# Performance work log

Hardware: AMD Instinct MI355X
Metric: run time of the kernel (lower is better)

The kernel has to match this reference:

```python
import jax, jax.numpy as jnp
import numpy as np

NW, NT, ND = 100000, 20000, 5000      # wallet / token / dev node counts
DW, DT, DD = 32, 32, 16               # raw feature dims
H = 64                                 # GATConv out channels (heads=1)
E_WW, E_BU, E_SE, E_CR = 1600000, 1000000, 1000000, 20000


def setup_inputs() -> dict:
    key = jax.random.key(0)
    ks = iter(jax.random.split(key, 80))

    def nrm(shape, s=1.0):
        return jax.random.normal(next(ks), shape, dtype=jnp.float32) * s

    inp = {
        "x_wallet": nrm((NW, DW)),
        "x_token": nrm((NT, DT)),
        "x_dev": nrm((ND, DD)),
    }
    # per-relation GATConv params: lin_src, lin_dst (bias=False), att_src, att_dst, bias
    rels = [("g1ww", DW, DW), ("g1bu", DW, DT), ("g1se", DW, DT), ("g1cr", DD, DT),
            ("g2ww", H, H), ("g2bu", H, H), ("g2se", H, H)]
    for pre, ds, dd in rels:
        inp[pre + "_Ws"] = nrm((ds, H), 0.1)
        inp[pre + "_Wd"] = nrm((dd, H), 0.1)
        inp[pre + "_as"] = nrm((H,), 0.1)
        inp[pre + "_ad"] = nrm((H,), 0.1)
        inp[pre + "_b"] = nrm((H,), 0.1)
    inp["Wfc"] = nrm((H, 2), 0.1)
    inp["bfc"] = nrm((2,), 0.1)

    for name, n, hi in [("ww_src", E_WW, NW), ("ww_dst", E_WW, NW),
                        ("bu_src", E_BU, NW), ("bu_dst", E_BU, NT),
                        ("se_src", E_SE, NW), ("se_dst", E_SE, NT),
                        ("cr_src", E_CR, ND), ("cr_dst", E_CR, NT)]:
        inp[name] = jax.random.randint(next(ks), (n,), 0, hi, dtype=jnp.int32)
    return inp


def gat(xs, xd, src, dst, Ws, Wd, a_s, a_d, b, n_dst):
    """PyG GATConv, heads=1, add_self_loops=False, negative_slope=0.2."""
    hs = xs @ Ws                                   # [Ns, H]
    e = jax.nn.leaky_relu((hs @ a_s)[src] + ((xd @ Wd) @ a_d)[dst], 0.2)  # [E]
    m = jax.ops.segment_max(e, dst, num_segments=n_dst)
    ex = jnp.exp(e - m[dst])
    den = jax.ops.segment_sum(ex, dst, num_segments=n_dst)
    alpha = ex / (den[dst] + 1e-16)                # scatter-softmax over dst
    out = jax.ops.segment_sum(alpha[:, None] * hs[src], dst, num_segments=n_dst)
    return out + b


def reference(x_wallet, x_token, x_dev,
              g1ww_Ws, g1ww_Wd, g1ww_as, g1ww_ad, g1ww_b,
              g1bu_Ws, g1bu_Wd, g1bu_as, g1bu_ad, g1bu_b,
              g1se_Ws, g1se_Wd, g1se_as, g1se_ad, g1se_b,
              g1cr_Ws, g1cr_Wd, g1cr_as, g1cr_ad, g1cr_b,
              g2ww_Ws, g2ww_Wd, g2ww_as, g2ww_ad, g2ww_b,
              g2bu_Ws, g2bu_Wd, g2bu_as, g2bu_ad, g2bu_b,
              g2se_Ws, g2se_Wd, g2se_as, g2se_ad, g2se_b,
              Wfc, bfc,
              ww_src, ww_dst, bu_src, bu_dst, se_src, se_dst, cr_src, cr_dst):
    # conv1 (HeteroConv, aggr='sum'): dev has no incoming edges -> dropped
    w1 = gat(x_wallet, x_wallet, ww_src, ww_dst, g1ww_Ws, g1ww_Wd, g1ww_as, g1ww_ad, g1ww_b, NW)
    t1 = (gat(x_wallet, x_token, bu_src, bu_dst, g1bu_Ws, g1bu_Wd, g1bu_as, g1bu_ad, g1bu_b, NT)
          + gat(x_wallet, x_token, se_src, se_dst, g1se_Ws, g1se_Wd, g1se_as, g1se_ad, g1se_b, NT)
          + gat(x_dev, x_token, cr_src, cr_dst, g1cr_Ws, g1cr_Wd, g1cr_as, g1cr_ad, g1cr_b, NT))
    # conv2: 'dev' absent from x_dict, so ('dev','creates','token') is skipped by HeteroConv
    w2 = gat(w1, w1, ww_src, ww_dst, g2ww_Ws, g2ww_Wd, g2ww_as, g2ww_ad, g2ww_b, NW)  # computed but unused downstream (matches torch)
    t2 = (gat(w1, t1, bu_src, bu_dst, g2bu_Ws, g2bu_Wd, g2bu_as, g2bu_ad, g2bu_b, NT)
          + gat(w1, t1, se_src, se_dst, g2se_Ws, g2se_Wd, g2se_as, g2se_ad, g2se_b, NT))
    del w2
    return t2 @ Wfc + bfc  # [NT, 2]
```

## Files before the change

kernel.cpp:

```cpp
#include <hip/hip_runtime.h>

#define NW 100000
#define NT 20000
#define ND 5000
#define EWW 1600000
#define EBU 1000000
#define ESE 1000000
#define ECR 20000
#define EPB 16384
#define SBTH 1024
#define SITER 16
#define ABTH 512

#define WWSH 8
#define WWW 256
#define NBWB 391
#define WCAP 6144
#define WITER 12
#define TSH 6
#define TW 64
#define NBTB 313
#define TCAP 4096
#define TITER 8
#define CCAP 512
#define CITER 1

typedef unsigned int uint;

#define R_EDWW 0
#define R_EDBU 1
#define R_EDSE 2
#define R_EDCR 3
#define R_WV2BU 4
#define R_WV2SE 5
#define R_ESWW 6
#define R_ESBU 7
#define R_ESSE 8
#define R_ESCR 9
#define R_WS2BU 10
#define R_WS2SE 11
#define R_VBU 12
#define R_VSE 13
#define R_DBU_B 14
#define R_DSE_B 15
#define R_DBU_S 16
#define R_DSE_S 17
#define R_DBU_C 18
#define R_DSE_C 19
#define R_TBU0 20
#define R_TBU1 21
#define R_TSE0 22
#define R_TSE1 23
#define R_CBU 24
#define R_CSE 25
#define R_SBU 26
#define R_SSE 27
#define R_MBU0 28
#define R_MBU1 29
#define R_MSE0 30
#define R_MSE1 31
#define R_CB1U0 32
#define R_CB1U1 33
#define R_CB1S0 34
#define R_CB1S1 35
#define R_C20 36
#define R_C21 37
#define R_F0 38
#define R_F1 39
#define R_BT1 40
#define R_BT2 41
#define NROWS 42


__global__ void k_scur(int* __restrict__ ccur) {
    int t = blockIdx.x * 256 + threadIdx.x;
    if (t < 4096) {
        int li = t >> 10, i = t & 1023;
        int cap = (li == 0) ? WCAP : (li == 3 ? CCAP : TCAP);
        ccur[t] = i * cap;
    }
}

__global__ __launch_bounds__(64) void k_smallprep(const float* __restrict__ Wfc,
                                                  const float* __restrict__ b1a,
                                                  const float* __restrict__ b1b,
                                                  const float* __restrict__ b1c,
                                                  const float* __restrict__ b2a,
                                                  const float* __restrict__ b2b,
                                                  float* __restrict__ wvbuf) {
    int t = threadIdx.x;
    if (blockIdx.x == 0) {
        wvbuf[R_F0 * 64 + t] = Wfc[t * 2];
        wvbuf[R_F1 * 64 + t] = Wfc[t * 2 + 1];
    } else if (blockIdx.x == 1) {
        wvbuf[R_BT1 * 64 + t] = b1a[t] + b1b[t] + b1c[t];
    } else {
        wvbuf[R_BT2 * 64 + t] = b2a[t] + b2b[t];
    }
}


struct BMeta {
    const int* src[4]; const int* dst[4];
    int* ccur[4];
    uint* pairs[4];
    int E[4]; int shift[4]; int cap[4]; int bbase[5];
};

__device__ __forceinline__ int find_list(const int* bbase, int b) {
    int li = 0;
    while (li < 3 && b >= bbase[li + 1]) ++li;
    return li;
}

__global__ __launch_bounds__(SBTH) void k_cscat4(BMeta a) {
    __shared__ int scnt[1024];
    __shared__ int sbase[1024];
    for (int i = threadIdx.x; i < 1024; i += SBTH) scnt[i] = 0;
    __syncthreads();
    int li = find_list(a.bbase, blockIdx.x);
    int lb = blockIdx.x - a.bbase[li];
    const int* src = a.src[li];
    const int* dst = a.dst[li];
    uint* pairs = a.pairs[li];
    int* ccur = a.ccur[li];
    int sh = a.shift[li];
    int cap = a.cap[li];
    uint mask = (1u << sh) - 1u;
    int b0 = lb * EPB;
    int end = min(b0 + EPB, a.E[li]);
    int t = threadIdx.x;

    uint pk[SITER];
    int bk[SITER];
    int rk[SITER];
#pragma unroll
    for (int k = 0; k < SITER; ++k) {
        int i = b0 + t + k * SBTH;
        bool v = i < end;
        int d = v ? dst[i] : 0;
        int s = v ? src[i] : 0;
        int b = d >> sh;
        pk[k] = (uint)s | (((uint)d & mask) << 20);
        rk[k] = v ? atomicAdd(&scnt[b], 1) : 0;
        bk[k] = v ? b : -1;
    }
    __syncthreads();
    for (int i = t; i < 1024; i += SBTH) {
        int c = scnt[i];
        sbase[i] = c ? atomicAdd(&ccur[i], c) : 0;
    }
    __syncthreads();
#pragma unroll
    for (int k = 0; k < SITER; ++k) {
        if (bk[k] >= 0) {
            int p = sbase[bk[k]] + rk[k];
            if (p < (bk[k] + 1) * cap)
                pairs[p] = pk[k];
        }
    }
}


struct WvN { const float* M[16]; const float* v[16]; int K[16]; };

__global__ __launch_bounds__(64) void k_wvN(WvN a, float* __restrict__ out) {
    int b = blockIdx.x, t = threadIdx.x;
    if (t < a.K[b]) {
        const float* M = a.M[b];
        const float* v = a.v[b];
        float s = 0.f;
        for (int j = 0; j < 64; ++j) s = fmaf(M[t * 64 + j], v[j], s);
        out[b * 64 + t] = s;
    }
}


struct PrepWP {
    const float* X; int N;
    const float* v[14];
    float* edww;
    float* PW; float4* TB; float4* TS;
};

__global__ __launch_bounds__(256) void k_prepw(PrepWP a) {
    int wvid = (blockIdx.x * 256 + threadIdx.x) >> 6;
    int half = (threadIdx.x >> 5) & 1;
    int l = threadIdx.x & 31;
    int r = wvid * 2 + half;
    float x = (r < a.N) ? a.X[(size_t)r * 32 + l] : 0.f;
    float p[14];
#pragma unroll
    for (int i = 0; i < 14; ++i) p[i] = x * a.v[i][l];
#pragma unroll
    for (int o = 1; o < 32; o <<= 1) {
#pragma unroll
        for (int i = 0; i < 14; ++i) p[i] += __shfl_xor(p[i], o, 64);
    }
    if (l == 0 && r < a.N) {
        a.edww[r] = p[3];
        float4* P = (float4*)(a.PW + (size_t)r * 8);
        P[0] = make_float4(p[4], p[5], p[6], p[7]);
        P[1] = make_float4(p[8], p[9], p[0], 0.f);
        a.TB[r] = make_float4(p[10], p[11], p[1], 0.f);
        a.TS[r] = make_float4(p[12], p[13], p[2], 0.f);
    }
}

struct PrepTD {
    const float* Xt; const float* Xd;
    const float* tv0; const float* tv1; const float* tv2;
    const float* dv0; const float* dv1; const float* dv2;
    float* e0; float* e1; float* e2;
    float4* TC;
    int nbT;
};

__global__ __launch_bounds__(256) void k_preptd(PrepTD a) {
    if ((int)blockIdx.x < a.nbT) {
        int wvid = (blockIdx.x * 256 + threadIdx.x) >> 6;
        int half = (threadIdx.x >> 5) & 1;
        int l = threadIdx.x & 31;
        int r = wvid * 2 + half;
        float x = (r < NT) ? a.Xt[(size_t)r * 32 + l] : 0.f;
        float p0 = x * a.tv0[l], p1 = x * a.tv1[l], p2 = x * a.tv2[l];
#pragma unroll
        for (int o = 1; o < 32; o <<= 1) {
            p0 += __shfl_xor(p0, o, 64);
            p1 += __shfl_xor(p1, o, 64);
            p2 += __shfl_xor(p2, o, 64);
        }
        if (l == 0 && r < NT) { a.e0[r] = p0; a.e1[r] = p1; a.e2[r] = p2; }
    } else {
        int grp = ((blockIdx.x - a.nbT) * 256 + threadIdx.x) >> 4;
        int l = threadIdx.x & 15;
        int r = grp;
        float x = (r < ND) ? a.Xd[(size_t)r * 16 + l] : 0.f;
        float p0 = x * a.dv0[l], p1 = x * a.dv1[l], p2 = x * a.dv2[l];
#pragma unroll
        for (int o = 1; o < 16; o <<= 1) {
            p0 += __shfl_xor(p0, o, 64);
            p1 += __shfl_xor(p1, o, 64);
            p2 += __shfl_xor(p2, o, 64);
        }
        if (l == 0 && r < ND) a.TC[r] = make_float4(p1, p2, p0, 0.f);
    }
}


template <int ITER>
__device__ __forceinline__ void sort_bucket(const uint* __restrict__ slab, int cnt,
                                            int ndl, uint* sp, int* hoff, int* hcnt,
                                            int t) {
    if (t < ndl) hcnt[t] = 0;
    __syncthreads();
    uint pk[ITER];
    int gk[ITER];
    int rk[ITER];
#pragma unroll
    for (int k = 0; k < ITER; ++k) {
        int i = t + k * ABTH;
        bool v = i < cnt;
        uint pr = v ? slab[i] : 0;
        int g = pr >> 20;
        pk[k] = pr & 0xFFFFFu;
        rk[k] = v ? atomicAdd(&hcnt[g], 1) : 0;
        gk[k] = v ? g : -1;
    }
    __syncthreads();
    int own = (t < ndl) ? hcnt[t] : 0;
    if (t < ndl) hoff[t] = own;
    __syncthreads();
    for (int o = 1; o < ndl; o <<= 1) {
        int u = 0;
        if (t < ndl && t >= o) u = hoff[t - o];
        __syncthreads();
        if (t < ndl && t >= o) hoff[t] += u;
        __syncthreads();
    }
    if (t < ndl) hoff[t] -= own;
    __syncthreads();
#pragma unroll
    for (int k = 0; k < ITER; ++k)
        if (gk[k] >= 0) sp[hoff[gk[k]] + rk[k]] = pk[k];
    __syncthreads();
}


__global__ __launch_bounds__(ABTH) void k_fsaggw(const uint* __restrict__ pairs,
                                                 const int* __restrict__ ccur,
                                                 const float* __restrict__ ed,
                                                 const float* __restrict__ PW,
                                                 const float* __restrict__ C,
                                                 float4* __restrict__ TL2B,
                                                 float4* __restrict__ TL2S) {
    __shared__ uint sp[WCAP];
    __shared__ int hoff[WWW];
    __shared__ int hcnt[WWW];
    __shared__ float eds[WWW];
    int t = threadIdx.x, b = blockIdx.x;
    int d0 = b << WWSH;
    if (t < WWW) {
        int d = d0 + t;
        eds[t] = (d < NW) ? ed[d] : 0.f;
    }
    int cnt = min(ccur[b] - b * WCAP, WCAP);
    sort_bucket<WITER>(pairs + (size_t)b * WCAP, cnt, WWW, sp, hoff, hcnt, t);
    int dl = t >> 1, sub = t & 1;
    float edj = eds[dl];
    float A0 = 0, A1 = 0, A2 = 0, A3 = 0, A4 = 0, A5 = 0, den = 0;
    int s0 = hoff[dl], s1 = s0 + hcnt[dl];
    for (int j = s0 + sub; j < s1; j += 2) {
        int s = sp[j];
        const float4* P = (const float4*)(PW + (size_t)s * 8);
        float4 u = P[0], v = P[1];
        float e = v.z + edj;
        e = e > 0.f ? e : 0.2f * e;
        float w = __expf(e);
        den += w;
        A0 = fmaf(w, u.x, A0); A1 = fmaf(w, u.y, A1); A2 = fmaf(w, u.z, A2);
        A3 = fmaf(w, u.w, A3); A4 = fmaf(w, v.x, A4); A5 = fmaf(w, v.y, A5);
    }
    A0 += __shfl_xor(A0, 1, 64); A1 += __shfl_xor(A1, 1, 64);
    A2 += __shfl_xor(A2, 1, 64); A3 += __shfl_xor(A3, 1, 64);
    A4 += __shfl_xor(A4, 1, 64); A5 += __shfl_xor(A5, 1, 64);
    den += __shfl_xor(den, 1, 64);
    if (sub == 0) {
        int d = d0 + dl;
        if (d < NW) {
            float c0 = C[R_CBU * 64], c1 = C[R_CSE * 64];
            float c2 = C[R_CB1U0 * 64], c3 = C[R_CB1U1 * 64];
            float c4 = C[R_CB1S0 * 64], c5 = C[R_CB1S1 * 64];
            if (den > 0.f) {
                float inv = 1.f / (den + 1e-16f);
                TL2B[d] = make_float4(A2 * inv + c2, A3 * inv + c3, A0 * inv + c0, 0.f);
                TL2S[d] = make_float4(A4 * inv + c4, A5 * inv + c5, A1 * inv + c1, 0.f);
            } else {
                TL2B[d] = make_float4(c2, c3, c0, 0.f);
                TL2S[d] = make_float4(c4, c5, c1, 0.f);
            }
        }
    }
}


__global__ __launch_bounds__(ABTH) void k_fsaggt(const uint* __restrict__ pB,
                                                 const uint* __restrict__ pS,
                                                 const uint* __restrict__ pC,
                                                 const int* __restrict__ curB,
                                                 const int* __restrict__ curS,
                                                 const int* __restrict__ curC,
                                                 const float* __restrict__ edB,
                                                 const float* __restrict__ edS,
                                                 const float* __restrict__ edC,
                                                 const float4* __restrict__ TB,
                                                 const float4* __restrict__ TS,
                                                 const float4* __restrict__ TC,
                                                 const float4* __restrict__ TL2B,
                                                 const float4* __restrict__ TL2S,
                                                 const float* __restrict__ C,
                                                 const float* __restrict__ bfc,
                                                 float* __restrict__ out) {
    __shared__ uint spB[TCAP];
    __shared__ uint spS[TCAP];
    __shared__ uint spC[CCAP];
    __shared__ int hoB[TW], hcB[TW], hoS[TW], hcS[TW], hoC[TW], hcC[TW];
    __shared__ float eds[3][TW];
    int t = threadIdx.x, b = blockIdx.x;
    int d0 = b << TSH;
    if (t < TW) {
        int d = d0 + t;
        eds[0][t] = (d < NT) ? edB[d] : 0.f;
        eds[1][t] = (d < NT) ? edS[d] : 0.f;
        eds[2][t] = (d < NT) ? edC[d] : 0.f;
    }
    int cntB = min(curB[b] - b * TCAP, TCAP);
    int cntS = min(curS[b] - b * TCAP, TCAP);
    int cntC = min(curC[b] - b * CCAP, CCAP);
    sort_bucket<TITER>(pB + (size_t)b * TCAP, cntB, TW, spB, hoB, hcB, t);
    sort_bucket<TITER>(pS + (size_t)b * TCAP, cntS, TW, spS, hoS, hcS, t);
    sort_bucket<CITER>(pC + (size_t)b * CCAP, cntC, TW, spC, hoC, hcC, t);

    int dl = t >> 3, sub = t & 7;

    float bx = 0, by = 0, bd = 0;
    for (int j = hoB[dl] + sub; j < hoB[dl] + hcB[dl]; j += 8) {
        float4 q = TB[spB[j]];
        float e = q.z + eds[0][dl];
        e = e > 0.f ? e : 0.2f * e;
        float w = __expf(e);
        bd += w; bx = fmaf(w, q.x, bx); by = fmaf(w, q.y, by);
    }
    float sx = 0, sy = 0, sd = 0;
    for (int j = hoS[dl] + sub; j < hoS[dl] + hcS[dl]; j += 8) {
        float4 q = TS[spS[j]];
        float e = q.z + eds[1][dl];
        e = e > 0.f ? e : 0.2f * e;
        float w = __expf(e);
        sd += w; sx = fmaf(w, q.x, sx); sy = fmaf(w, q.y, sy);
    }
    float cx = 0, cy = 0, cd = 0;
    for (int j = hoC[dl] + sub; j < hoC[dl] + hcC[dl]; j += 8) {
        float4 q = TC[spC[j]];
        float e = q.z + eds[2][dl];
        e = e > 0.f ? e : 0.2f * e;
        float w = __expf(e);
        cd += w; cx = fmaf(w, q.x, cx); cy = fmaf(w, q.y, cy);
    }
#pragma unroll
    for (int o = 1; o < 8; o <<= 1) {
        bx += __shfl_xor(bx, o, 64); by += __shfl_xor(by, o, 64); bd += __shfl_xor(bd, o, 64);
        sx += __shfl_xor(sx, o, 64); sy += __shfl_xor(sy, o, 64); sd += __shfl_xor(sd, o, 64);
        cx += __shfl_xor(cx, o, 64); cy += __shfl_xor(cy, o, 64); cd += __shfl_xor(cd, o, 64);
    }
    float qbx = 0, qby = 0, qsx = 0, qsy = 0, qcx = 0, qcy = 0;
    if (bd > 0.f) { float i = 1.f / (bd + 1e-16f); qbx = bx * i; qby = by * i; }
    if (sd > 0.f) { float i = 1.f / (sd + 1e-16f); qsx = sx * i; qsy = sy * i; }
    if (cd > 0.f) { float i = 1.f / (cd + 1e-16f); qcx = cx * i; qcy = cy * i; }
    float ed2b = C[R_SBU * 64] + qbx + qsx + qcx;
    float ed2s = C[R_SSE * 64] + qby + qsy + qcy;

    float rbx = 0, rby = 0, rbd = 0;
    for (int j = hoB[dl] + sub; j < hoB[dl] + hcB[dl]; j += 8) {
        float4 q = TL2B[spB[j]];
        float e = q.z + ed2b;
        e = e > 0.f ? e : 0.2f * e;
        float w = __expf(e);
        rbd += w; rbx = fmaf(w, q.x, rbx); rby = fmaf(w, q.y, rby);
    }
    float rsx = 0, rsy = 0, rsd = 0;
    for (int j = hoS[dl] + sub; j < hoS[dl] + hcS[dl]; j += 8) {
        float4 q = TL2S[spS[j]];
        float e = q.z + ed2s;
        e = e > 0.f ? e : 0.2f * e;
        float w = __expf(e);
        rsd += w; rsx = fmaf(w, q.x, rsx); rsy = fmaf(w, q.y, rsy);
    }
#pragma unroll
    for (int o = 1; o < 8; o <<= 1) {
        rbx += __shfl_xor(rbx, o, 64); rby += __shfl_xor(rby, o, 64); rbd += __shfl_xor(rbd, o, 64);
        rsx += __shfl_xor(rsx, o, 64); rsy += __shfl_xor(rsy, o, 64); rsd += __shfl_xor(rsd, o, 64);
    }
    if (sub == 0) {
        int d = d0 + dl;
        if (d < NT) {
            float fbx = 0, fby = 0, fsx = 0, fsy = 0;
            if (rbd > 0.f) { float i = 1.f / (rbd + 1e-16f); fbx = rbx * i; fby = rby * i; }
            if (rsd > 0.f) { float i = 1.f / (rsd + 1e-16f); fsx = rsx * i; fsy = rsy * i; }
            out[d * 2 + 0] = bfc[0] + C[R_C20 * 64] + fbx + fsx;
            out[d * 2 + 1] = bfc[1] + C[R_C21 * 64] + fby + fsy;
        }
    }
}


extern "C" void kernel_launch(void* const* d_in, const int* in_sizes, int n_in,
                              void* d_out, int out_size, void* d_ws, size_t ws_size,
                              hipStream_t stream) {
    const float* xw = (const float*)d_in[0];
    const float* xt = (const float*)d_in[1];
    const float* xd = (const float*)d_in[2];
    const float* g1ww_Ws = (const float*)d_in[3];
    const float* g1ww_Wd = (const float*)d_in[4];
    const float* g1ww_as = (const float*)d_in[5];
    const float* g1ww_ad = (const float*)d_in[6];
    const float* g1ww_b  = (const float*)d_in[7];
    const float* g1bu_Ws = (const float*)d_in[8];
    const float* g1bu_Wd = (const float*)d_in[9];
    const float* g1bu_as = (const float*)d_in[10];
    const float* g1bu_ad = (const float*)d_in[11];
    const float* g1bu_b  = (const float*)d_in[12];
    const float* g1se_Ws = (const float*)d_in[13];
    const float* g1se_Wd = (const float*)d_in[14];
    const float* g1se_as = (const float*)d_in[15];
    const float* g1se_ad = (const float*)d_in[16];
    const float* g1se_b  = (const float*)d_in[17];
    const float* g1cr_Ws = (const float*)d_in[18];
    const float* g1cr_Wd = (const float*)d_in[19];
    const float* g1cr_as = (const float*)d_in[20];
    const float* g1cr_ad = (const float*)d_in[21];
    const float* g1cr_b  = (const float*)d_in[22];
    const float* g2bu_Ws = (const float*)d_in[28];
    const float* g2bu_Wd = (const float*)d_in[29];
    const float* g2bu_as = (const float*)d_in[30];
    const float* g2bu_ad = (const float*)d_in[31];
    const float* g2bu_b  = (const float*)d_in[32];
    const float* g2se_Ws = (const float*)d_in[33];
    const float* g2se_Wd = (const float*)d_in[34];
    const float* g2se_as = (const float*)d_in[35];
    const float* g2se_ad = (const float*)d_in[36];
    const float* g2se_b  = (const float*)d_in[37];
    const float* Wfc = (const float*)d_in[38];
    const float* bfc = (const float*)d_in[39];
    const int* ww_src = (const int*)d_in[40];
    const int* ww_dst = (const int*)d_in[41];
    const int* bu_src = (const int*)d_in[42];
    const int* bu_dst = (const int*)d_in[43];
    const int* se_src = (const int*)d_in[44];
    const int* se_dst = (const int*)d_in[45];
    const int* cr_src = (const int*)d_in[46];
    const int* cr_dst = (const int*)d_in[47];

    char* p = (char*)d_ws;
    auto alloc = [&](size_t bytes) {
        char* r = p;
        p += (bytes + 255) & ~(size_t)255;
        return r;
    };
    uint* pairsW = (uint*)alloc((size_t)NBWB * WCAP * 4);
    uint* pairsB = (uint*)alloc((size_t)NBTB * TCAP * 4);
    uint* pairsS = (uint*)alloc((size_t)NBTB * TCAP * 4);
    uint* pairsC = (uint*)alloc((size_t)NBTB * CCAP * 4);
    int* ccur = (int*)alloc(4 * 1024 * 4);

    float* wvbuf = (float*)alloc(NROWS * 64 * 4);

    float* edww = (float*)alloc((size_t)NW * 4);
    float* edbu = (float*)alloc((size_t)NT * 4);
    float* edse = (float*)alloc((size_t)NT * 4);
    float* edcr = (float*)alloc((size_t)NT * 4);
    float* PW   = (float*)alloc((size_t)NW * 8 * 4);
    float4* TB  = (float4*)alloc((size_t)NW * 16);
    float4* TS  = (float4*)alloc((size_t)NW * 16);
    float4* TC  = (float4*)alloc((size_t)ND * 16);
    float4* TL2B = (float4*)alloc((size_t)NW * 16);
    float4* TL2S = (float4*)alloc((size_t)NW * 16);

    const int thr = 256;
    const int nbW_e = (EWW + EPB - 1) / EPB;
    const int nbB_e = (EBU + EPB - 1) / EPB;
    const int nbS_e = (ESE + EPB - 1) / EPB;
    const int nbC_e = (ECR + EPB - 1) / EPB;
    const int nbTot = nbW_e + nbB_e + nbS_e + nbC_e;

    k_scur<<<16, thr, 0, stream>>>(ccur);

    BMeta bm;
    bm.src[0] = ww_src; bm.dst[0] = ww_dst; bm.ccur[0] = ccur + 0 * 1024;
    bm.pairs[0] = pairsW; bm.E[0] = EWW; bm.shift[0] = WWSH; bm.cap[0] = WCAP;
    bm.src[1] = bu_src; bm.dst[1] = bu_dst; bm.ccur[1] = ccur + 1 * 1024;
    bm.pairs[1] = pairsB; bm.E[1] = EBU; bm.shift[1] = TSH; bm.cap[1] = TCAP;
    bm.src[2] = se_src; bm.dst[2] = se_dst; bm.ccur[2] = ccur + 2 * 1024;
    bm.pairs[2] = pairsS; bm.E[2] = ESE; bm.shift[2] = TSH; bm.cap[2] = TCAP;
    bm.src[3] = cr_src; bm.dst[3] = cr_dst; bm.ccur[3] = ccur + 3 * 1024;
    bm.pairs[3] = pairsC; bm.E[3] = ECR; bm.shift[3] = TSH; bm.cap[3] = CCAP;
    bm.bbase[0] = 0; bm.bbase[1] = nbW_e; bm.bbase[2] = nbW_e + nbB_e;
    bm.bbase[3] = nbW_e + nbB_e + nbS_e; bm.bbase[4] = nbTot;
    k_cscat4<<<nbTot, SBTH, 0, stream>>>(bm);

    k_smallprep<<<3, 64, 0, stream>>>(Wfc, g1bu_b, g1se_b, g1cr_b, g2bu_b, g2se_b, wvbuf);

    WvN A;
    A.M[0] = g1ww_Wd; A.v[0] = g1ww_ad; A.K[0] = 32;
    A.M[1] = g1bu_Wd; A.v[1] = g1bu_ad; A.K[1] = 32;
    A.M[2] = g1se_Wd; A.v[2] = g1se_ad; A.K[2] = 32;
    A.M[3] = g1cr_Wd; A.v[3] = g1cr_ad; A.K[3] = 32;
    A.M[4] = g2bu_Wd; A.v[4] = g2bu_ad; A.K[4] = 64;
    A.M[5] = g2se_Wd; A.v[5] = g2se_ad; A.K[5] = 64;
    A.M[6] = g1ww_Ws; A.v[6] = g1ww_as; A.K[6] = 32;
    A.M[7] = g1bu_Ws; A.v[7] = g1bu_as; A.K[7] = 32;
    A.M[8] = g1se_Ws; A.v[8] = g1se_as; A.K[8] = 32;
    A.M[9] = g1cr_Ws; A.v[9] = g1cr_as; A.K[9] = 16;
    A.M[10] = g2bu_Ws; A.v[10] = g2bu_as; A.K[10] = 64;
    A.M[11] = g2se_Ws; A.v[11] = g2se_as; A.K[11] = 64;
    for (int i = 12; i < 16; ++i) { A.M[i] = nullptr; A.v[i] = nullptr; A.K[i] = 0; }
    k_wvN<<<12, 64, 0, stream>>>(A, wvbuf + 0 * 64);

    WvN B;
    B.M[0] = g1ww_Ws; B.v[0] = wvbuf + R_WS2BU * 64; B.K[0] = 32;
    B.M[1] = g1ww_Ws; B.v[1] = wvbuf + R_WS2SE * 64; B.K[1] = 32;
    B.M[2] = g1bu_Ws; B.v[2] = wvbuf + R_WV2BU * 64; B.K[2] = 32;
    B.M[3] = g1bu_Ws; B.v[3] = wvbuf + R_WV2SE * 64; B.K[3] = 32;
    B.M[4] = g1se_Ws; B.v[4] = wvbuf + R_WV2BU * 64; B.K[4] = 32;
    B.M[5] = g1se_Ws; B.v[5] = wvbuf + R_WV2SE * 64; B.K[5] = 32;
    B.M[6] = g1cr_Ws; B.v[6] = wvbuf + R_WV2BU * 64; B.K[6] = 16;
    B.M[7] = g1cr_Ws; B.v[7] = wvbuf + R_WV2SE * 64; B.K[7] = 16;
    B.M[8] = g2bu_Ws; B.v[8] = wvbuf + R_F0 * 64; B.K[8] = 64;
    B.M[9] = g2bu_Ws; B.v[9] = wvbuf + R_F1 * 64; B.K[9] = 64;
    B.M[10] = g2se_Ws; B.v[10] = wvbuf + R_F0 * 64; B.K[10] = 64;
    B.M[11] = g2se_Ws; B.v[11] = wvbuf + R_F1 * 64; B.K[11] = 64;
    B.M[12] = g1ww_b; B.v[12] = wvbuf + R_WS2BU * 64; B.K[12] = 1;
    B.M[13] = g1ww_b; B.v[13] = wvbuf + R_WS2SE * 64; B.K[13] = 1;
    B.M[14] = wvbuf + R_BT1 * 64; B.v[14] = wvbuf + R_WV2BU * 64; B.K[14] = 1;
    B.M[15] = wvbuf + R_BT1 * 64; B.v[15] = wvbuf + R_WV2SE * 64; B.K[15] = 1;
    k_wvN<<<16, 64, 0, stream>>>(B, wvbuf + R_VBU * 64);

    WvN Cc;
    Cc.M[0] = g1ww_Ws; Cc.v[0] = wvbuf + R_TBU0 * 64; Cc.K[0] = 32;
    Cc.M[1] = g1ww_Ws; Cc.v[1] = wvbuf + R_TBU1 * 64; Cc.K[1] = 32;
    Cc.M[2] = g1ww_Ws; Cc.v[2] = wvbuf + R_TSE0 * 64; Cc.K[2] = 32;
    Cc.M[3] = g1ww_Ws; Cc.v[3] = wvbuf + R_TSE1 * 64; Cc.K[3] = 32;
    Cc.M[4] = g1ww_b; Cc.v[4] = wvbuf + R_TBU0 * 64; Cc.K[4] = 1;
    Cc.M[5] = g1ww_b; Cc.v[5] = wvbuf + R_TBU1 * 64; Cc.K[5] = 1;
    Cc.M[6] = g1ww_b; Cc.v[6] = wvbuf + R_TSE0 * 64; Cc.K[6] = 1;
    Cc.M[7] = g1ww_b; Cc.v[7] = wvbuf + R_TSE1 * 64; Cc.K[7] = 1;
    Cc.M[8] = wvbuf + R_BT2 * 64; Cc.v[8] = wvbuf + R_F0 * 64; Cc.K[8] = 1;
    Cc.M[9] = wvbuf + R_BT2 * 64; Cc.v[9] = wvbuf + R_F1 * 64; Cc.K[9] = 1;
    for (int i = 10; i < 16; ++i) { Cc.M[i] = nullptr; Cc.v[i] = nullptr; Cc.K[i] = 0; }
    k_wvN<<<10, 64, 0, stream>>>(Cc, wvbuf + R_MBU0 * 64);

    PrepWP pw;
    pw.X = xw; pw.N = NW;
    pw.v[0] = wvbuf + R_ESWW * 64; pw.v[1] = wvbuf + R_ESBU * 64;
    pw.v[2] = wvbuf + R_ESSE * 64; pw.v[3] = wvbuf + R_EDWW * 64;
    pw.v[4] = wvbuf + R_VBU * 64;  pw.v[5] = wvbuf + R_VSE * 64;
    pw.v[6] = wvbuf + R_MBU0 * 64; pw.v[7] = wvbuf + R_MBU1 * 64;
    pw.v[8] = wvbuf + R_MSE0 * 64; pw.v[9] = wvbuf + R_MSE1 * 64;
    pw.v[10] = wvbuf + R_DBU_B * 64; pw.v[11] = wvbuf + R_DSE_B * 64;
    pw.v[12] = wvbuf + R_DBU_S * 64; pw.v[13] = wvbuf + R_DSE_S * 64;
    pw.edww = edww;
    pw.PW = PW; pw.TB = TB; pw.TS = TS;
    k_prepw<<<(NW + 7) / 8, thr, 0, stream>>>(pw);

    PrepTD ptd;
    ptd.Xt = xt; ptd.Xd = xd;
    ptd.tv0 = wvbuf + R_EDBU * 64; ptd.tv1 = wvbuf + R_EDSE * 64; ptd.tv2 = wvbuf + R_EDCR * 64;
    ptd.dv0 = wvbuf + R_ESCR * 64; ptd.dv1 = wvbuf + R_DBU_C * 64; ptd.dv2 = wvbuf + R_DSE_C * 64;
    ptd.e0 = edbu; ptd.e1 = edse; ptd.e2 = edcr;
    ptd.TC = TC;
    ptd.nbT = (NT + 7) / 8;
    k_preptd<<<ptd.nbT + (ND + 15) / 16, thr, 0, stream>>>(ptd);

    k_fsaggw<<<NBWB, ABTH, 0, stream>>>(pairsW, ccur + 0 * 1024, edww, PW, wvbuf,
                                        TL2B, TL2S);

    k_fsaggt<<<NBTB, ABTH, 0, stream>>>(pairsB, pairsS, pairsC,
                                        ccur + 1 * 1024, ccur + 2 * 1024, ccur + 3 * 1024,
                                        edbu, edse, edcr,
                                        TB, TS, TC, TL2B, TL2S,
                                        wvbuf, bfc, (float*)d_out);
}
```

Measured before the change: 295.9 us.

## Fuse init kernels and merge edge scatter with node prep into one launch

Result: faster. 273.6 us (-7.6%).

```diff
diff --git a/kernel.cpp b/kernel.cpp
--- a/kernel.cpp
+++ b/kernel.cpp
@@ -8,7 +8,7 @@
 #define ESE 1000000
 #define ECR 20000
 #define EPB 16384
-#define SBTH 1024
+#define BBTH 1024
 #define SITER 16
 #define ABTH 512
 
@@ -71,98 +71,46 @@
 #define R_BT2 41
 #define NROWS 42
 
-
-__global__ void k_scur(int* __restrict__ ccur) {
-    int t = blockIdx.x * 256 + threadIdx.x;
-    if (t < 4096) {
-        int li = t >> 10, i = t & 1023;
+struct WvN { const float* M[16]; const float* v[16]; int K[16]; };
+
+
+struct Init1 {
+    WvN A;
+    const float* Wfc;
+    const float* b1a; const float* b1b; const float* b1c;
+    const float* b2a; const float* b2b;
+    int* ccur;
+    float* wvbuf;
+};
+
+__global__ __launch_bounds__(256) void k_init1(Init1 a) {
+    int bi = blockIdx.x, t = threadIdx.x;
+    if (bi < 16) {
+        int i = bi * 256 + t;
+        int li = i >> 10, j = i & 1023;
         int cap = (li == 0) ? WCAP : (li == 3 ? CCAP : TCAP);
-        ccur[t] = i * cap;
-    }
-}
-
-__global__ __launch_bounds__(64) void k_smallprep(const float* __restrict__ Wfc,
-                                                  const float* __restrict__ b1a,
-                                                  const float* __restrict__ b1b,
-                                                  const float* __restrict__ b1c,
-                                                  const float* __restrict__ b2a,
-                                                  const float* __restrict__ b2b,
-                                                  float* __restrict__ wvbuf) {
-    int t = threadIdx.x;
-    if (blockIdx.x == 0) {
-        wvbuf[R_F0 * 64 + t] = Wfc[t * 2];
-        wvbuf[R_F1 * 64 + t] = Wfc[t * 2 + 1];
-    } else if (blockIdx.x == 1) {
-        wvbuf[R_BT1 * 64 + t] = b1a[t] + b1b[t] + b1c[t];
+        a.ccur[i] = j * cap;
+    } else if (bi == 16) {
+        if (t < 64) {
+            a.wvbuf[R_F0 * 64 + t] = a.Wfc[t * 2];
+            a.wvbuf[R_F1 * 64 + t] = a.Wfc[t * 2 + 1];
+        }
+    } else if (bi == 17) {
+        if (t < 64) a.wvbuf[R_BT1 * 64 + t] = a.b1a[t] + a.b1b[t] + a.b1c[t];
+    } else if (bi == 18) {
+        if (t < 64) a.wvbuf[R_BT2 * 64 + t] = a.b2a[t] + a.b2b[t];
     } else {
-        wvbuf[R_BT2 * 64 + t] = b2a[t] + b2b[t];
-    }
-}
-
-
-struct BMeta {
-    const int* src[4]; const int* dst[4];
-    int* ccur[4];
-    uint* pairs[4];
-    int E[4]; int shift[4]; int cap[4]; int bbase[5];
-};
-
-__device__ __forceinline__ int find_list(const int* bbase, int b) {
-    int li = 0;
-    while (li < 3 && b >= bbase[li + 1]) ++li;
-    return li;
-}
-
-__global__ __launch_bounds__(SBTH) void k_cscat4(BMeta a) {
-    __shared__ int scnt[1024];
-    __shared__ int sbase[1024];
-    for (int i = threadIdx.x; i < 1024; i += SBTH) scnt[i] = 0;
-    __syncthreads();
-    int li = find_list(a.bbase, blockIdx.x);
-    int lb = blockIdx.x - a.bbase[li];
-    const int* src = a.src[li];
-    const int* dst = a.dst[li];
-    uint* pairs = a.pairs[li];
-    int* ccur = a.ccur[li];
-    int sh = a.shift[li];
-    int cap = a.cap[li];
-    uint mask = (1u << sh) - 1u;
-    int b0 = lb * EPB;
-    int end = min(b0 + EPB, a.E[li]);
-    int t = threadIdx.x;
-
-    uint pk[SITER];
-    int bk[SITER];
-    int rk[SITER];
-#pragma unroll
-    for (int k = 0; k < SITER; ++k) {
-        int i = b0 + t + k * SBTH;
-        bool v = i < end;
-        int d = v ? dst[i] : 0;
-        int s = v ? src[i] : 0;
-        int b = d >> sh;
-        pk[k] = (uint)s | (((uint)d & mask) << 20);
-        rk[k] = v ? atomicAdd(&scnt[b], 1) : 0;
-        bk[k] = v ? b : -1;
-    }
-    __syncthreads();
-    for (int i = t; i < 1024; i += SBTH) {
-        int c = scnt[i];
-        sbase[i] = c ? atomicAdd(&ccur[i], c) : 0;
-    }
-    __syncthreads();
-#pragma unroll
-    for (int k = 0; k < SITER; ++k) {
-        if (bk[k] >= 0) {
-            int p = sbase[bk[k]] + rk[k];
-            if (p < (bk[k] + 1) * cap)
-                pairs[p] = pk[k];
-        }
-    }
-}
-
-
-struct WvN { const float* M[16]; const float* v[16]; int K[16]; };
+        int b = bi - 19;
+        if (t < a.A.K[b]) {
+            const float* M = a.A.M[b];
+            const float* v = a.A.v[b];
+            float s = 0.f;
+            for (int j = 0; j < 64; ++j) s = fmaf(M[t * 64 + j], v[j], s);
+            a.wvbuf[b * 64 + t] = s;
+        }
+    }
+}
+
 
 __global__ __launch_bounds__(64) void k_wvN(WvN a, float* __restrict__ out) {
     int b = blockIdx.x, t = threadIdx.x;
@@ -176,51 +124,106 @@
 }
 
 
-struct PrepWP {
-    const float* X; int N;
-    const float* v[14];
-    float* edww;
-    float* PW; float4* TB; float4* TS;
+struct BMeta {
+    const int* src[4]; const int* dst[4];
+    int* ccur[4];
+    uint* pairs[4];
+    int E[4]; int shift[4]; int cap[4]; int bbase[5];
 };
 
-__global__ __launch_bounds__(256) void k_prepw(PrepWP a) {
-    int wvid = (blockIdx.x * 256 + threadIdx.x) >> 6;
-    int half = (threadIdx.x >> 5) & 1;
-    int l = threadIdx.x & 31;
-    int r = wvid * 2 + half;
-    float x = (r < a.N) ? a.X[(size_t)r * 32 + l] : 0.f;
-    float p[14];
-#pragma unroll
-    for (int i = 0; i < 14; ++i) p[i] = x * a.v[i][l];
-#pragma unroll
-    for (int o = 1; o < 32; o <<= 1) {
-#pragma unroll
-        for (int i = 0; i < 14; ++i) p[i] += __shfl_xor(p[i], o, 64);
-    }
-    if (l == 0 && r < a.N) {
-        a.edww[r] = p[3];
-        float4* P = (float4*)(a.PW + (size_t)r * 8);
-        P[0] = make_float4(p[4], p[5], p[6], p[7]);
-        P[1] = make_float4(p[8], p[9], p[0], 0.f);
-        a.TB[r] = make_float4(p[10], p[11], p[1], 0.f);
-        a.TS[r] = make_float4(p[12], p[13], p[2], 0.f);
-    }
-}
-
-struct PrepTD {
+struct Build {
+    BMeta bm;
+    const float* Xw;
+    const float* vw[14];
+    float* edww; float* PW; float4* TBt; float4* TSt;
     const float* Xt; const float* Xd;
     const float* tv0; const float* tv1; const float* tv2;
     const float* dv0; const float* dv1; const float* dv2;
     float* e0; float* e1; float* e2;
     float4* TC;
-    int nbT;
+    int nbScat, nbPW, nbPT;
 };
 
-__global__ __launch_bounds__(256) void k_preptd(PrepTD a) {
-    if ((int)blockIdx.x < a.nbT) {
-        int wvid = (blockIdx.x * 256 + threadIdx.x) >> 6;
-        int half = (threadIdx.x >> 5) & 1;
-        int l = threadIdx.x & 31;
+__device__ __forceinline__ int find_list(const int* bbase, int b) {
+    int li = 0;
+    while (li < 3 && b >= bbase[li + 1]) ++li;
+    return li;
+}
+
+__global__ __launch_bounds__(BBTH) void k_build(Build a) {
+    int t = threadIdx.x;
+    if ((int)blockIdx.x < a.nbScat) {
+        __shared__ int scnt[1024];
+        __shared__ int sbase[1024];
+        for (int i = t; i < 1024; i += BBTH) scnt[i] = 0;
+        __syncthreads();
+        int li = find_list(a.bm.bbase, blockIdx.x);
+        int lb = blockIdx.x - a.bm.bbase[li];
+        const int* src = a.bm.src[li];
+        const int* dst = a.bm.dst[li];
+        uint* pairs = a.bm.pairs[li];
+        int* ccur = a.bm.ccur[li];
+        int sh = a.bm.shift[li];
+        int cap = a.bm.cap[li];
+        uint mask = (1u << sh) - 1u;
+        int b0 = lb * EPB;
+        int end = min(b0 + EPB, a.bm.E[li]);
+        uint pk[SITER];
+        int bk[SITER];
+        int rk[SITER];
+#pragma unroll
+        for (int k = 0; k < SITER; ++k) {
+            int i = b0 + t + k * BBTH;
+            bool v = i < end;
+            int d = v ? dst[i] : 0;
+            int s = v ? src[i] : 0;
+            int b = d >> sh;
+            pk[k] = (uint)s | (((uint)d & mask) << 20);
+            rk[k] = v ? atomicAdd(&scnt[b], 1) : 0;
+            bk[k] = v ? b : -1;
+        }
+        __syncthreads();
+        for (int i = t; i < 1024; i += BBTH) {
+            int c = scnt[i];
+            sbase[i] = c ? atomicAdd(&ccur[i], c) : 0;
+        }
+        __syncthreads();
+#pragma unroll
+        for (int k = 0; k < SITER; ++k) {
+            if (bk[k] >= 0) {
+                int p = sbase[bk[k]] + rk[k];
+                if (p < (bk[k] + 1) * cap)
+                    pairs[p] = pk[k];
+            }
+        }
+    } else if ((int)blockIdx.x < a.nbScat + a.nbPW) {
+        int bid = blockIdx.x - a.nbScat;
+        int wvid = (bid * BBTH + t) >> 6;
+        int half = (t >> 5) & 1;
+        int l = t & 31;
+        int r = wvid * 2 + half;
+        float x = (r < NW) ? a.Xw[(size_t)r * 32 + l] : 0.f;
+        float p[14];
+#pragma unroll
+        for (int i = 0; i < 14; ++i) p[i] = x * a.vw[i][l];
+#pragma unroll
+        for (int o = 1; o < 32; o <<= 1) {
+#pragma unroll
+            for (int i = 0; i < 14; ++i) p[i] += __shfl_xor(p[i], o, 64);
+        }
+        if (l == 0 && r < NW) {
+            a.edww[r] = p[3];
+            float4* P = (float4*)(a.PW + (size_t)r * 8);
+            P[0] = make_float4(p[4], p[5], p[6], p[7]);
+            P[1] = make_float4(p[8], p[9], p[0], 0.f);
+            a.TBt[r] = make_float4(p[10], p[11], p[1], 0.f);
+            a.TSt[r] = make_float4(p[12], p[13], p[2], 0.f);
+        }
+    } else if ((int)blockIdx.x < a.nbScat + a.nbPW + a.nbPT) {
+        int bid = blockIdx.x - a.nbScat - a.nbPW;
+        int wvid = (bid * BBTH + t) >> 6;
+        int half = (t >> 5) & 1;
+        int l = t & 31;
         int r = wvid * 2 + half;
         float x = (r < NT) ? a.Xt[(size_t)r * 32 + l] : 0.f;
         float p0 = x * a.tv0[l], p1 = x * a.tv1[l], p2 = x * a.tv2[l];
@@ -232,9 +235,9 @@
         }
         if (l == 0 && r < NT) { a.e0[r] = p0; a.e1[r] = p1; a.e2[r] = p2; }
     } else {
-        int grp = ((blockIdx.x - a.nbT) * 256 + threadIdx.x) >> 4;
-        int l = threadIdx.x & 15;
-        int r = grp;
+        int bid = blockIdx.x - a.nbScat - a.nbPW - a.nbPT;
+        int r = (bid * BBTH + t) >> 4;
+        int l = t & 15;
         float x = (r < ND) ? a.Xd[(size_t)r * 16 + l] : 0.f;
         float p0 = x * a.dv0[l], p1 = x * a.dv1[l], p2 = x * a.dv2[l];
 #pragma unroll
@@ -526,45 +529,35 @@
     float4* TL2B = (float4*)alloc((size_t)NW * 16);
     float4* TL2S = (float4*)alloc((size_t)NW * 16);
 
-    const int thr = 256;
     const int nbW_e = (EWW + EPB - 1) / EPB;
     const int nbB_e = (EBU + EPB - 1) / EPB;
     const int nbS_e = (ESE + EPB - 1) / EPB;
     const int nbC_e = (ECR + EPB - 1) / EPB;
-    const int nbTot = nbW_e + nbB_e + nbS_e + nbC_e;
-
-    k_scur<<<16, thr, 0, stream>>>(ccur);
-
-    BMeta bm;
-    bm.src[0] = ww_src; bm.dst[0] = ww_dst; bm.ccur[0] = ccur + 0 * 1024;
-    bm.pairs[0] = pairsW; bm.E[0] = EWW; bm.shift[0] = WWSH; bm.cap[0] = WCAP;
-    bm.src[1] = bu_src; bm.dst[1] = bu_dst; bm.ccur[1] = ccur + 1 * 1024;
-    bm.pairs[1] = pairsB; bm.E[1] = EBU; bm.shift[1] = TSH; bm.cap[1] = TCAP;
-    bm.src[2] = se_src; bm.dst[2] = se_dst; bm.ccur[2] = ccur + 2 * 1024;
-    bm.pairs[2] = pairsS; bm.E[2] = ESE; bm.shift[2] = TSH; bm.cap[2] = TCAP;
-    bm.src[3] = cr_src; bm.dst[3] = cr_dst; bm.ccur[3] = ccur + 3 * 1024;
-    bm.pairs[3] = pairsC; bm.E[3] = ECR; bm.shift[3] = TSH; bm.cap[3] = CCAP;
-    bm.bbase[0] = 0; bm.bbase[1] = nbW_e; bm.bbase[2] = nbW_e + nbB_e;
-    bm.bbase[3] = nbW_e + nbB_e + nbS_e; bm.bbase[4] = nbTot;
-    k_cscat4<<<nbTot, SBTH, 0, stream>>>(bm);
-
-    k_smallprep<<<3, 64, 0, stream>>>(Wfc, g1bu_b, g1se_b, g1cr_b, g2bu_b, g2se_b, wvbuf);
-
-    WvN A;
-    A.M[0] = g1ww_Wd; A.v[0] = g1ww_ad; A.K[0] = 32;
-    A.M[1] = g1bu_Wd; A.v[1] = g1bu_ad; A.K[1] = 32;
-    A.M[2] = g1se_Wd; A.v[2] = g1se_ad; A.K[2] = 32;
-    A.M[3] = g1cr_Wd; A.v[3] = g1cr_ad; A.K[3] = 32;
-    A.M[4] = g2bu_Wd; A.v[4] = g2bu_ad; A.K[4] = 64;
-    A.M[5] = g2se_Wd; A.v[5] = g2se_ad; A.K[5] = 64;
-    A.M[6] = g1ww_Ws; A.v[6] = g1ww_as; A.K[6] = 32;
-    A.M[7] = g1bu_Ws; A.v[7] = g1bu_as; A.K[7] = 32;
-    A.M[8] = g1se_Ws; A.v[8] = g1se_as; A.K[8] = 32;
-    A.M[9] = g1cr_Ws; A.v[9] = g1cr_as; A.K[9] = 16;
-    A.M[10] = g2bu_Ws; A.v[10] = g2bu_as; A.K[10] = 64;
-    A.M[11] = g2se_Ws; A.v[11] = g2se_as; A.K[11] = 64;
-    for (int i = 12; i < 16; ++i) { A.M[i] = nullptr; A.v[i] = nullptr; A.K[i] = 0; }
-    k_wvN<<<12, 64, 0, stream>>>(A, wvbuf + 0 * 64);
+    const int nbScat = nbW_e + nbB_e + nbS_e + nbC_e;
+    const int nbPW = (NW + 31) / 32;
+    const int nbPT = (NT + 31) / 32;
+    const int nbPD = (ND + 63) / 64;
+
+    Init1 i1;
+    i1.A.M[0] = g1ww_Wd; i1.A.v[0] = g1ww_ad; i1.A.K[0] = 32;
+    i1.A.M[1] = g1bu_Wd; i1.A.v[1] = g1bu_ad; i1.A.K[1] = 32;
+    i1.A.M[2] = g1se_Wd; i1.A.v[2] = g1se_ad; i1.A.K[2] = 32;
+    i1.A.M[3] = g1cr_Wd; i1.A.v[3] = g1cr_ad; i1.A.K[3] = 32;
+    i1.A.M[4] = g2bu_Wd; i1.A.v[4] = g2bu_ad; i1.A.K[4] = 64;
+    i1.A.M[5] = g2se_Wd; i1.A.v[5] = g2se_ad; i1.A.K[5] = 64;
+    i1.A.M[6] = g1ww_Ws; i1.A.v[6] = g1ww_as; i1.A.K[6] = 32;
+    i1.A.M[7] = g1bu_Ws; i1.A.v[7] = g1bu_as; i1.A.K[7] = 32;
+    i1.A.M[8] = g1se_Ws; i1.A.v[8] = g1se_as; i1.A.K[8] = 32;
+    i1.A.M[9] = g1cr_Ws; i1.A.v[9] = g1cr_as; i1.A.K[9] = 16;
+    i1.A.M[10] = g2bu_Ws; i1.A.v[10] = g2bu_as; i1.A.K[10] = 64;
+    i1.A.M[11] = g2se_Ws; i1.A.v[11] = g2se_as; i1.A.K[11] = 64;
+    for (int i = 12; i < 16; ++i) { i1.A.M[i] = nullptr; i1.A.v[i] = nullptr; i1.A.K[i] = 0; }
+    i1.Wfc = Wfc;
+    i1.b1a = g1bu_b; i1.b1b = g1se_b; i1.b1c = g1cr_b;
+    i1.b2a = g2bu_b; i1.b2b = g2se_b;
+    i1.ccur = ccur;
+    i1.wvbuf = wvbuf;
+    k_init1<<<31, 256, 0, stream>>>(i1);
 
     WvN B;
     B.M[0] = g1ww_Ws; B.v[0] = wvbuf + R_WS2BU * 64; B.K[0] = 32;
@@ -599,27 +592,33 @@
     for (int i = 10; i < 16; ++i) { Cc.M[i] = nullptr; Cc.v[i] = nullptr; Cc.K[i] = 0; }
     k_wvN<<<10, 64, 0, stream>>>(Cc, wvbuf + R_MBU0 * 64);
 
-    PrepWP pw;
-    pw.X = xw; pw.N = NW;
-    pw.v[0] = wvbuf + R_ESWW * 64; pw.v[1] = wvbuf + R_ESBU * 64;
-    pw.v[2] = wvbuf + R_ESSE * 64; pw.v[3] = wvbuf + R_EDWW * 64;
-    pw.v[4] = wvbuf + R_VBU * 64;  pw.v[5] = wvbuf + R_VSE * 64;
-    pw.v[6] = wvbuf + R_MBU0 * 64; pw.v[7] = wvbuf + R_MBU1 * 64;
-    pw.v[8] = wvbuf + R_MSE0 * 64; pw.v[9] = wvbuf + R_MSE1 * 64;
-    pw.v[10] = wvbuf + R_DBU_B * 64; pw.v[11] = wvbuf + R_DSE_B * 64;
-    pw.v[12] = wvbuf + R_DBU_S * 64; pw.v[13] = wvbuf + R_DSE_S * 64;
-    pw.edww = edww;
-    pw.PW = PW; pw.TB = TB; pw.TS = TS;
-    k_prepw<<<(NW + 7) / 8, thr, 0, stream>>>(pw);
-
-    PrepTD ptd;
-    ptd.Xt = xt; ptd.Xd = xd;
-    ptd.tv0 = wvbuf + R_EDBU * 64; ptd.tv1 = wvbuf + R_EDSE * 64; ptd.tv2 = wvbuf + R_EDCR * 64;
-    ptd.dv0 = wvbuf + R_ESCR * 64; ptd.dv1 = wvbuf + R_DBU_C * 64; ptd.dv2 = wvbuf + R_DSE_C * 64;
-    ptd.e0 = edbu; ptd.e1 = edse; ptd.e2 = edcr;
-    ptd.TC = TC;
-    ptd.nbT = (NT + 7) / 8;
-    k_preptd<<<ptd.nbT + (ND + 15) / 16, thr, 0, stream>>>(ptd);
+    Build bd;
+    bd.bm.src[0] = ww_src; bd.bm.dst[0] = ww_dst; bd.bm.ccur[0] = ccur + 0 * 1024;
+    bd.bm.pairs[0] = pairsW; bd.bm.E[0] = EWW; bd.bm.shift[0] = WWSH; bd.bm.cap[0] = WCAP;
+    bd.bm.src[1] = bu_src; bd.bm.dst[1] = bu_dst; bd.bm.ccur[1] = ccur + 1 * 1024;
+    bd.bm.pairs[1] = pairsB; bd.bm.E[1] = EBU; bd.bm.shift[1] = TSH; bd.bm.cap[1] = TCAP;
+    bd.bm.src[2] = se_src; bd.bm.dst[2] = se_dst; bd.bm.ccur[2] = ccur + 2 * 1024;
+    bd.bm.pairs[2] = pairsS; bd.bm.E[2] = ESE; bd.bm.shift[2] = TSH; bd.bm.cap[2] = TCAP;
+    bd.bm.src[3] = cr_src; bd.bm.dst[3] = cr_dst; bd.bm.ccur[3] = ccur + 3 * 1024;
+    bd.bm.pairs[3] = pairsC; bd.bm.E[3] = ECR; bd.bm.shift[3] = TSH; bd.bm.cap[3] = CCAP;
+    bd.bm.bbase[0] = 0; bd.bm.bbase[1] = nbW_e; bd.bm.bbase[2] = nbW_e + nbB_e;
+    bd.bm.bbase[3] = nbW_e + nbB_e + nbS_e; bd.bm.bbase[4] = nbScat;
+    bd.Xw = xw;
+    bd.vw[0] = wvbuf + R_ESWW * 64; bd.vw[1] = wvbuf + R_ESBU * 64;
+    bd.vw[2] = wvbuf + R_ESSE * 64; bd.vw[3] = wvbuf + R_EDWW * 64;
+    bd.vw[4] = wvbuf + R_VBU * 64;  bd.vw[5] = wvbuf + R_VSE * 64;
+    bd.vw[6] = wvbuf + R_MBU0 * 64; bd.vw[7] = wvbuf + R_MBU1 * 64;
+    bd.vw[8] = wvbuf + R_MSE0 * 64; bd.vw[9] = wvbuf + R_MSE1 * 64;
+    bd.vw[10] = wvbuf + R_DBU_B * 64; bd.vw[11] = wvbuf + R_DSE_B * 64;
+    bd.vw[12] = wvbuf + R_DBU_S * 64; bd.vw[13] = wvbuf + R_DSE_S * 64;
+    bd.edww = edww; bd.PW = PW; bd.TBt = TB; bd.TSt = TS;
+    bd.Xt = xt; bd.Xd = xd;
+    bd.tv0 = wvbuf + R_EDBU * 64; bd.tv1 = wvbuf + R_EDSE * 64; bd.tv2 = wvbuf + R_EDCR * 64;
+    bd.dv0 = wvbuf + R_ESCR * 64; bd.dv1 = wvbuf + R_DBU_C * 64; bd.dv2 = wvbuf + R_DSE_C * 64;
+    bd.e0 = edbu; bd.e1 = edse; bd.e2 = edcr;
+    bd.TC = TC;
+    bd.nbScat = nbScat; bd.nbPW = nbPW; bd.nbPT = nbPT;
+    k_build<<<nbScat + nbPW + nbPT + nbPD, BBTH, 0, stream>>>(bd);
 
     k_fsaggw<<<NBWB, ABTH, 0, stream>>>(pairsW, ccur + 0 * 1024, edww, PW, wvbuf,
                                         TL2B, TL2S);
```
